# Performance work log

Hardware: AMD Instinct MI355X
Metric: run time of the kernel (lower is better)

Reference implementation:

```python
import jax, jax.numpy as jnp
import numpy as np

CODE_DIMS = [32, 32, 16]   # prod = 16384 out features
FEAT_DIM = 1024
EPS = 1e-6


def setup_inputs() -> dict:
    key = jax.random.key(0)
    kx, kw = jax.random.split(key)
    x = jax.random.normal(kx, (4, 2048, FEAT_DIM), dtype=jnp.float32)
    # per-chunk trunc-normal init like _init_weights: std = sqrt(2/(feat_dim+code_dim)), clipped at +-3 std
    parts = []
    for i, cd in enumerate(CODE_DIMS):
        std = float(np.sqrt(2.0 / (FEAT_DIM + cd)))
        parts.append(std * jax.random.truncated_normal(
            jax.random.fold_in(kw, i), -3.0, 3.0, (cd, FEAT_DIM), dtype=jnp.float32))
    weight = jnp.concatenate(parts, axis=0)  # (sum(code_dims)=80, feat_dim)
    return {"x": x, "weight": weight}


def _rms_norm(y):
    var = jnp.mean(y * y, axis=-1, keepdims=True) + EPS
    return y * jax.lax.rsqrt(var)


def reference(x, weight):
    # split weight rows into the low-rank factors
    a, b, c = jnpp_split = jnp.split(weight, np.cumsum(CODE_DIMS)[:-1].tolist(), axis=0)
    # outer product over code dims, shared feature axis z -> dynamic weight (prod(code_dims), feat_dim)
    W = jnp.einsum('az,bz,cz->abcz', a, b, c).reshape(-1, weight.shape[-1])
    y = jnp.einsum('bsi,oi->bso', x, W)  # dense projection
    return _rms_norm(y)
```

## Files before the change

### kernel.cpp

```cpp
#include <hip/hip_runtime.h>
#include <hip/hip_bf16.h>

typedef unsigned short u16;
typedef __attribute__((ext_vector_type(8))) short bf16x8;
typedef __attribute__((ext_vector_type(4))) float f32x4;
typedef __attribute__((ext_vector_type(8))) unsigned short ushort8;

#define FEAT 1024
#define NOUT 16384
#define EPS 1e-6f
#define NT 16

#define GLOBAL_AS __attribute__((address_space(1)))
#define LDS_AS __attribute__((address_space(3)))

__device__ __forceinline__ void load16_to_lds(const u16* g, u16* l) {
    __builtin_amdgcn_global_load_lds((const GLOBAL_AS void*)g, (LDS_AS void*)l, 16, 0, 0);
}

__device__ __forceinline__ u16 f32_to_bf16_bits(float f) {
    __hip_bfloat16 h = __float2bfloat16(f);
    return *reinterpret_cast<u16*>(&h);
}

__device__ __forceinline__ float bf16_bits_to_f32(u16 b) {
    unsigned u = ((unsigned)b) << 16;
    float f;
    __builtin_memcpy(&f, &u, 4);
    return f;
}

__global__ void wbuild_kernel(const float* __restrict__ w, u16* __restrict__ Wb) {
    const int t  = blockIdx.x * 256 + threadIdx.x;
    const int p  = t >> 7;
    const int k0 = (t & 127) << 3;
    const int o  = (p & ~63) | ((p & 15) << 2) | ((p >> 4) & 3);
    const int ai = o >> 9;
    const int bi = (o >> 4) & 31;
    const int ci = o & 15;
    const float* A = w + ai * FEAT + k0;
    const float* B = w + (32 + bi) * FEAT + k0;
    const float* C = w + (64 + ci) * FEAT + k0;
    ushort8 r;
#pragma unroll
    for (int j = 0; j < 8; ++j) r[j] = f32_to_bf16_bits(A[j] * B[j] * C[j]);
    *reinterpret_cast<ushort8*>(Wb + (size_t)t * 8) = r;
}

__global__ void xcast_kernel(const float* __restrict__ x, u16* __restrict__ Xb) {
    const int t = blockIdx.x * 256 + threadIdx.x;
    const float4* xv = reinterpret_cast<const float4*>(x) + (size_t)t * 2;
    const float4 f0 = xv[0];
    const float4 f1 = xv[1];
    float vals[8] = {f0.x, f0.y, f0.z, f0.w, f1.x, f1.y, f1.z, f1.w};
    ushort8 r;
#pragma unroll
    for (int j = 0; j < 8; ++j) r[j] = f32_to_bf16_bits(vals[j]);
    *reinterpret_cast<ushort8*>(Xb + (size_t)t * 8) = r;
}


#define LDSOFF(buf, isB, kh) (((buf) << 15) + ((isB) << 14) + ((kh) << 13))

#define STAGE(isB, tt, kh, buf) do {                                          \
    const u16* g = ((isB) ? gB : gA) + (size_t)(tt) * 64 + (kh) * 32 + w * 32768; \
    u16* l = lds + LDSOFF(buf, isB, kh) + w * 1024;                           \
    load16_to_lds(g, l);                                                      \
    load16_to_lds(g + 16384, l + 512);                                        \
} while (0)

#define RD_A(dst, mi, ks, buf) dst = *reinterpret_cast<const bf16x8*>(        \
    lds + LDSOFF(buf, 0, ks) + (wm * 128 + (mi) * 16 + fr) * 32 + ((kg ^ ((fr >> 1) & 3)) << 3))
#define RD_B(dst, nj, ks, buf) dst = *reinterpret_cast<const bf16x8*>(        \
    lds + LDSOFF(buf, 1, ks) + (wn * 64 + (nj) * 16 + fr) * 32 + ((kg ^ ((fr >> 1) & 3)) << 3))

#define BAR() do {                                                            \
    __builtin_amdgcn_sched_barrier(0);                                        \
    __builtin_amdgcn_s_barrier();                                             \
    __builtin_amdgcn_sched_barrier(0);                                        \
} while (0)

#define MFMAQ(mibase) do {                                                    \
    __builtin_amdgcn_s_setprio(1);                                            \
    _Pragma("unroll")                                                         \
    for (int mi = 0; mi < 4; ++mi) {                                          \
        acc[(mibase)+mi][0] = __builtin_amdgcn_mfma_f32_16x16x32_bf16(a[mi], b[0], acc[(mibase)+mi][0], 0, 0, 0); \
        acc[(mibase)+mi][1] = __builtin_amdgcn_mfma_f32_16x16x32_bf16(a[mi], b[1], acc[(mibase)+mi][1], 0, 0, 0); \
        acc[(mibase)+mi][2] = __builtin_amdgcn_mfma_f32_16x16x32_bf16(a[mi], b[2], acc[(mibase)+mi][2], 0, 0, 0); \
        acc[(mibase)+mi][3] = __builtin_amdgcn_mfma_f32_16x16x32_bf16(a[mi], b[3], acc[(mibase)+mi][3], 0, 0, 0); \
    }                                                                         \
    __builtin_amdgcn_s_setprio(0);                                            \
} while (0)

#define WAIT_H1(t) do {                                                       \
    if ((t) == NT - 1) { asm volatile("s_waitcnt vmcnt(0)" ::: "memory"); }   \
    else               { asm volatile("s_waitcnt vmcnt(8)" ::: "memory"); }   \
} while (0)
#define WAIT_H2(t) do {                                                       \
    if ((t) < NT - 2)       { asm volatile("s_waitcnt vmcnt(8)" ::: "memory"); } \
    else if ((t) == NT - 2) { asm volatile("s_waitcnt vmcnt(4)" ::: "memory"); } \
} while (0)

#define HALF(kh, buf, doStage, stT, stKh, stBuf, WAITC) do {                  \
    RD_A(a[0], 0, kh, buf); RD_A(a[1], 1, kh, buf);                           \
    RD_A(a[2], 2, kh, buf); RD_A(a[3], 3, kh, buf);                           \
    RD_B(b[0], 0, kh, buf); RD_B(b[1], 1, kh, buf);                           \
    RD_B(b[2], 2, kh, buf); RD_B(b[3], 3, kh, buf);                           \
    if (doStage) STAGE(0, stT, stKh, stBuf);                                  \
    MFMAQ(0);                                                                 \
    RD_A(a[0], 4, kh, buf); RD_A(a[1], 5, kh, buf);                           \
    RD_A(a[2], 6, kh, buf); RD_A(a[3], 7, kh, buf);                           \
    if (doStage) STAGE(1, stT, stKh, stBuf);                                  \
    MFMAQ(4);                                                                 \
    WAITC;                                                                    \
    BAR();                                                                    \
} while (0)

#define TILE_BODY(t, buf, nbuf) do {                                          \
    HALF(0, buf, (t) < NT - 1, (t) + 1, 1, nbuf, WAIT_H1(t));                 \
    HALF(1, buf, (t) < NT - 2, (t) + 2, 0, buf,  WAIT_H2(t));                 \
} while (0)

__global__ __launch_bounds__(512, 2) void gemm_kernel(const u16* __restrict__ Xb,
                                                      const u16* __restrict__ Wb,
                                                      u16* __restrict__ Y) {
    __shared__ u16 lds[65536];

    const int tid  = threadIdx.x;
    const int lane = tid & 63;
    const int w    = tid >> 6;
    const int wm   = w >> 2;
    const int wn   = w & 3;
    const int fr   = lane & 15;
    const int kg   = lane >> 4;

    const int bid = blockIdx.x;
    const int xcd = bid & 7;
    const int o   = bid >> 3;
    const int cb  = xcd * 8 + (o >> 7) * 4 + (o & 3);
    const int rb  = (o >> 2) & 31;
    const int brow = rb * 256;
    const int bcol = cb * 256;

    const int srow   = lane >> 2;
    const int kchunk = (lane & 3) ^ ((lane >> 3) & 3);
    const u16* gA = Xb + (size_t)(brow + srow) * FEAT + kchunk * 8;
    const u16* gB = Wb + (size_t)(bcol + srow) * FEAT + kchunk * 8;

    f32x4 acc[8][4] = {};
    bf16x8 a[4], b[4];

    STAGE(0, 0, 0, 0);
    STAGE(1, 0, 0, 0);
    STAGE(0, 0, 1, 0);
    STAGE(1, 0, 1, 0);
    STAGE(0, 1, 0, 1);
    STAGE(1, 1, 0, 1);
    asm volatile("s_waitcnt vmcnt(8)" ::: "memory");
    BAR();

    for (int tt = 0; tt < NT; tt += 2) {
        TILE_BODY(tt, 0, 1);
        TILE_BODY(tt + 1, 1, 0);
    }

    const int colbase = bcol + wn * 64 + fr * 4;
#pragma unroll
    for (int mi = 0; mi < 8; ++mi) {
#pragma unroll
        for (int r = 0; r < 4; ++r) {
            const int row = brow + wm * 128 + mi * 16 + kg * 4 + r;
            const unsigned lo = (unsigned)f32_to_bf16_bits(acc[mi][0][r]) |
                                ((unsigned)f32_to_bf16_bits(acc[mi][1][r]) << 16);
            const unsigned hi = (unsigned)f32_to_bf16_bits(acc[mi][2][r]) |
                                ((unsigned)f32_to_bf16_bits(acc[mi][3][r]) << 16);
            uint2 pk; pk.x = lo; pk.y = hi;
            *reinterpret_cast<uint2*>(Y + (size_t)row * 32768 + colbase) = pk;
        }
    }
}

__global__ __launch_bounds__(1024) void scale_kernel(const u16* __restrict__ Y,
                                                     float* __restrict__ out) {
    const int row = blockIdx.x;
    const int tid = threadIdx.x;
    const ushort8* yr = reinterpret_cast<const ushort8*>(Y + (size_t)row * 32768);
    const ushort8 v0 = yr[2 * tid];
    const ushort8 v1 = yr[2 * tid + 1];

    float f[16];
#pragma unroll
    for (int j = 0; j < 8; ++j) {
        f[j]     = bf16_bits_to_f32(v0[j]);
        f[8 + j] = bf16_bits_to_f32(v1[j]);
    }
    float ss = 0.f;
#pragma unroll
    for (int j = 0; j < 16; ++j) ss += f[j] * f[j];

#pragma unroll
    for (int off = 1; off < 64; off <<= 1) ss += __shfl_xor(ss, off, 64);
    __shared__ float wss[16];
    if ((tid & 63) == 0) wss[tid >> 6] = ss;
    __syncthreads();
    float tot = 0.f;
#pragma unroll
    for (int i = 0; i < 16; ++i) tot += wss[i];
    const float sc = rsqrtf(tot * (1.0f / (float)NOUT) + EPS);

    float4* orow = reinterpret_cast<float4*>(out + (size_t)row * NOUT) + tid * 4;
#pragma unroll
    for (int q = 0; q < 4; ++q) {
        float4 ov;
        ov.x = f[q * 4 + 0] * sc;
        ov.y = f[q * 4 + 1] * sc;
        ov.z = f[q * 4 + 2] * sc;
        ov.w = f[q * 4 + 3] * sc;
        orow[q] = ov;
    }
}

extern "C" void kernel_launch(void* const* d_in, const int* in_sizes, int n_in,
                              void* d_out, int out_size, void* d_ws, size_t ws_size,
                              hipStream_t stream) {
    const float* x = (const float*)d_in[0];
    const float* w = (const float*)d_in[1];
    float* out = (float*)d_out;

    const int M = in_sizes[0] / FEAT;

    u16* Wb = (u16*)d_ws;
    u16* Xb = (u16*)((char*)d_ws + (size_t)NOUT * FEAT * 2);

    u16* Y = (u16*)d_out;

    wbuild_kernel<<<(NOUT * (FEAT / 8)) / 256, 256, 0, stream>>>(w, Wb);
    xcast_kernel<<<(M * FEAT / 8) / 256, 256, 0, stream>>>(x, Xb);

    const int nblk = (M / 256) * (NOUT / 256);
    gemm_kernel<<<nblk, 512, 0, stream>>>(Xb, Wb, Y);

    scale_kernel<<<M, 1024, 0, stream>>>(Y, out);
}
```

Before: 451.7 us.

## Switch GEMM inner loop from 16x16x32 to 32x32x16 MFMA tiles

Replaces the 16x16x32 bf16 MFMA with the 32x32x16 variant. Each wave now holds 4x2 accumulators of 16 floats instead of 8x4 of 4, and fewer A/B fragments are read from LDS per step. The weight-row permutation in the build kernel and the epilogue store mapping change to match the new output layout. The aim is higher operand reuse per LDS read and fewer MFMA issues. The trade-off is narrower 4-byte stores in the epilogue and possible changes to LDS bank behaviour.

```diff
diff --git a/kernel.cpp b/kernel.cpp
--- a/kernel.cpp
+++ b/kernel.cpp
@@ -3,7 +3,7 @@
 
 typedef unsigned short u16;
 typedef __attribute__((ext_vector_type(8))) short bf16x8;
-typedef __attribute__((ext_vector_type(4))) float f32x4;
+typedef __attribute__((ext_vector_type(16))) float f32x16;
 typedef __attribute__((ext_vector_type(8))) unsigned short ushort8;
 
 #define FEAT 1024
@@ -34,7 +34,7 @@
     const int t  = blockIdx.x * 256 + threadIdx.x;
     const int p  = t >> 7;
     const int k0 = (t & 127) << 3;
-    const int o  = (p & ~63) | ((p & 15) << 2) | ((p >> 4) & 3);
+    const int o  = (p & ~63) | ((p & 31) << 1) | ((p >> 5) & 1);
     const int ai = o >> 9;
     const int bi = (o >> 4) & 31;
     const int ci = o & 15;
@@ -69,10 +69,12 @@
     load16_to_lds(g + 16384, l + 512);                                        \
 } while (0)
 
-#define RD_A(dst, mi, ks, buf) dst = *reinterpret_cast<const bf16x8*>(        \
-    lds + LDSOFF(buf, 0, ks) + (wm * 128 + (mi) * 16 + fr) * 32 + ((kg ^ ((fr >> 1) & 3)) << 3))
-#define RD_B(dst, nj, ks, buf) dst = *reinterpret_cast<const bf16x8*>(        \
-    lds + LDSOFF(buf, 1, ks) + (wn * 64 + (nj) * 16 + fr) * 32 + ((kg ^ ((fr >> 1) & 3)) << 3))
+#define RD_A(dst, mi, ks, kh, buf) dst = *reinterpret_cast<const bf16x8*>(    \
+    lds + LDSOFF(buf, 0, kh) + (wm * 128 + (mi) * 32 + fr5) * 32 +            \
+    (((((ks) * 2) + hi) ^ ((fr5 >> 1) & 3)) << 3))
+#define RD_B(dst, nt, ks, kh, buf) dst = *reinterpret_cast<const bf16x8*>(    \
+    lds + LDSOFF(buf, 1, kh) + (wn * 64 + (nt) * 32 + fr5) * 32 +             \
+    (((((ks) * 2) + hi) ^ ((fr5 >> 1) & 3)) << 3))
 
 #define BAR() do {                                                            \
     __builtin_amdgcn_sched_barrier(0);                                        \
@@ -80,14 +82,12 @@
     __builtin_amdgcn_sched_barrier(0);                                        \
 } while (0)
 
-#define MFMAQ(mibase) do {                                                    \
+#define MFMAQ() do {                                                          \
     __builtin_amdgcn_s_setprio(1);                                            \
     _Pragma("unroll")                                                         \
     for (int mi = 0; mi < 4; ++mi) {                                          \
-        acc[(mibase)+mi][0] = __builtin_amdgcn_mfma_f32_16x16x32_bf16(a[mi], b[0], acc[(mibase)+mi][0], 0, 0, 0); \
-        acc[(mibase)+mi][1] = __builtin_amdgcn_mfma_f32_16x16x32_bf16(a[mi], b[1], acc[(mibase)+mi][1], 0, 0, 0); \
-        acc[(mibase)+mi][2] = __builtin_amdgcn_mfma_f32_16x16x32_bf16(a[mi], b[2], acc[(mibase)+mi][2], 0, 0, 0); \
-        acc[(mibase)+mi][3] = __builtin_amdgcn_mfma_f32_16x16x32_bf16(a[mi], b[3], acc[(mibase)+mi][3], 0, 0, 0); \
+        acc[mi][0] = __builtin_amdgcn_mfma_f32_32x32x16_bf16(a[mi], b[0], acc[mi][0], 0, 0, 0); \
+        acc[mi][1] = __builtin_amdgcn_mfma_f32_32x32x16_bf16(a[mi], b[1], acc[mi][1], 0, 0, 0); \
     }                                                                         \
     __builtin_amdgcn_s_setprio(0);                                            \
 } while (0)
@@ -102,16 +102,16 @@
 } while (0)
 
 #define HALF(kh, buf, doStage, stT, stKh, stBuf, WAITC) do {                  \
-    RD_A(a[0], 0, kh, buf); RD_A(a[1], 1, kh, buf);                           \
-    RD_A(a[2], 2, kh, buf); RD_A(a[3], 3, kh, buf);                           \
-    RD_B(b[0], 0, kh, buf); RD_B(b[1], 1, kh, buf);                           \
-    RD_B(b[2], 2, kh, buf); RD_B(b[3], 3, kh, buf);                           \
+    RD_A(a[0], 0, 0, kh, buf); RD_A(a[1], 1, 0, kh, buf);                     \
+    RD_A(a[2], 2, 0, kh, buf); RD_A(a[3], 3, 0, kh, buf);                     \
+    RD_B(b[0], 0, 0, kh, buf); RD_B(b[1], 1, 0, kh, buf);                     \
     if (doStage) STAGE(0, stT, stKh, stBuf);                                  \
-    MFMAQ(0);                                                                 \
-    RD_A(a[0], 4, kh, buf); RD_A(a[1], 5, kh, buf);                           \
-    RD_A(a[2], 6, kh, buf); RD_A(a[3], 7, kh, buf);                           \
+    MFMAQ();                                                                  \
+    RD_A(a[0], 0, 1, kh, buf); RD_A(a[1], 1, 1, kh, buf);                     \
+    RD_A(a[2], 2, 1, kh, buf); RD_A(a[3], 3, 1, kh, buf);                     \
+    RD_B(b[0], 0, 1, kh, buf); RD_B(b[1], 1, 1, kh, buf);                     \
     if (doStage) STAGE(1, stT, stKh, stBuf);                                  \
-    MFMAQ(4);                                                                 \
+    MFMAQ();                                                                  \
     WAITC;                                                                    \
     BAR();                                                                    \
 } while (0)
@@ -131,8 +131,8 @@
     const int w    = tid >> 6;
     const int wm   = w >> 2;
     const int wn   = w & 3;
-    const int fr   = lane & 15;
-    const int kg   = lane >> 4;
+    const int fr5  = lane & 31;
+    const int hi   = lane >> 5;
 
     const int bid = blockIdx.x;
     const int xcd = bid & 7;
@@ -147,8 +147,8 @@
     const u16* gA = Xb + (size_t)(brow + srow) * FEAT + kchunk * 8;
     const u16* gB = Wb + (size_t)(bcol + srow) * FEAT + kchunk * 8;
 
-    f32x4 acc[8][4] = {};
-    bf16x8 a[4], b[4];
+    f32x16 acc[4][2] = {};
+    bf16x8 a[4], b[2];
 
     STAGE(0, 0, 0, 0);
     STAGE(1, 0, 0, 0);
@@ -164,18 +164,15 @@
         TILE_BODY(tt + 1, 1, 0);
     }
 
-    const int colbase = bcol + wn * 64 + fr * 4;
-#pragma unroll
-    for (int mi = 0; mi < 8; ++mi) {
-#pragma unroll
-        for (int r = 0; r < 4; ++r) {
-            const int row = brow + wm * 128 + mi * 16 + kg * 4 + r;
-            const unsigned lo = (unsigned)f32_to_bf16_bits(acc[mi][0][r]) |
-                                ((unsigned)f32_to_bf16_bits(acc[mi][1][r]) << 16);
-            const unsigned hi = (unsigned)f32_to_bf16_bits(acc[mi][2][r]) |
-                                ((unsigned)f32_to_bf16_bits(acc[mi][3][r]) << 16);
-            uint2 pk; pk.x = lo; pk.y = hi;
-            *reinterpret_cast<uint2*>(Y + (size_t)row * 32768 + colbase) = pk;
+    const int colbase = bcol + wn * 64 + fr5 * 2;
+#pragma unroll
+    for (int mi = 0; mi < 4; ++mi) {
+#pragma unroll
+        for (int rg = 0; rg < 16; ++rg) {
+            const int row = brow + wm * 128 + mi * 32 + (rg & 3) + 8 * (rg >> 2) + 4 * hi;
+            const unsigned pk = (unsigned)f32_to_bf16_bits(acc[mi][0][rg]) |
+                                ((unsigned)f32_to_bf16_bits(acc[mi][1][rg]) << 16);
+            *reinterpret_cast<unsigned*>(Y + (size_t)row * 32768 + colbase) = pk;
         }
     }
 }
```

Result: slower. 465.1 us (+3.0%).

## Load GEMM B operand directly from global into registers, bypassing LDS

Applied to the files above, without the earlier changes.

The weight (B) tiles are now read by each wave straight from global memory into registers with vector loads and double-buffered across k-halves. Only the X (A) tiles are still staged through LDS, so the LDS footprint is halved. The pipeline is rebuilt around this, with per-tile LDS staging of A and register prefetch of B ahead of the MFMAs. This removes LDS write/read traffic for B. In exchange, global-load latency now sits directly in front of the MFMAs, and B rows are fetched redundantly by the two wm wave groups through the cache.

```diff
diff --git a/kernel.cpp b/kernel.cpp
--- a/kernel.cpp
+++ b/kernel.cpp
@@ -60,19 +60,29 @@
 }
 
 
-#define LDSOFF(buf, isB, kh) (((buf) << 15) + ((isB) << 14) + ((kh) << 13))
-
-#define STAGE(isB, tt, kh, buf) do {                                          \
-    const u16* g = ((isB) ? gB : gA) + (size_t)(tt) * 64 + (kh) * 32 + w * 32768; \
-    u16* l = lds + LDSOFF(buf, isB, kh) + w * 1024;                           \
-    load16_to_lds(g, l);                                                      \
-    load16_to_lds(g + 16384, l + 512);                                        \
-} while (0)
-
-#define RD_A(dst, mi, ks, buf) dst = *reinterpret_cast<const bf16x8*>(        \
-    lds + LDSOFF(buf, 0, ks) + (wm * 128 + (mi) * 16 + fr) * 32 + ((kg ^ ((fr >> 1) & 3)) << 3))
-#define RD_B(dst, nj, ks, buf) dst = *reinterpret_cast<const bf16x8*>(        \
-    lds + LDSOFF(buf, 1, ks) + (wn * 64 + (nj) * 16 + fr) * 32 + ((kg ^ ((fr >> 1) & 3)) << 3))
+#define LOFF(buf, kh) ((buf) * 16384 + (kh) * 8192)
+
+#define STAGE_A(tt, buf) do {                                                 \
+    const u16* g = gA + (size_t)(tt) * 64 + (size_t)w * 32768;                \
+    u16* l0 = lds + LOFF(buf, 0) + w * 1024;                                  \
+    u16* l1 = lds + LOFF(buf, 1) + w * 1024;                                  \
+    load16_to_lds(g,             l0);                                         \
+    load16_to_lds(g + 16384,     l0 + 512);                                   \
+    load16_to_lds(g + 32,        l1);                                         \
+    load16_to_lds(g + 32 + 16384, l1 + 512);                                  \
+} while (0)
+
+#define LD_B(dst, tt, kh) do {                                                \
+    const u16* gb = gB + (size_t)(tt) * 64 + (kh) * 32;                       \
+    dst[0] = *reinterpret_cast<const bf16x8*>(gb);                            \
+    dst[1] = *reinterpret_cast<const bf16x8*>(gb + 16 * FEAT);                \
+    dst[2] = *reinterpret_cast<const bf16x8*>(gb + 32 * FEAT);                \
+    dst[3] = *reinterpret_cast<const bf16x8*>(gb + 48 * FEAT);                \
+} while (0)
+
+#define RD_A(dst, mi, mh, kh, buf) dst = *reinterpret_cast<const bf16x8*>(    \
+    lds + LOFF(buf, kh) + (wm * 128 + (mh) * 64 + (mi) * 16 + fr) * 32 +      \
+    ((kg ^ ((fr >> 1) & 3)) << 3))
 
 #define BAR() do {                                                            \
     __builtin_amdgcn_sched_barrier(0);                                        \
@@ -80,51 +90,51 @@
     __builtin_amdgcn_sched_barrier(0);                                        \
 } while (0)
 
-#define MFMAQ(mibase) do {                                                    \
+#define MFMAQ(mh, kh, buf, bb) do {                                           \
+    bf16x8 a0, a1, a2, a3;                                                    \
+    RD_A(a0, 0, mh, kh, buf); RD_A(a1, 1, mh, kh, buf);                       \
+    RD_A(a2, 2, mh, kh, buf); RD_A(a3, 3, mh, kh, buf);                       \
     __builtin_amdgcn_s_setprio(1);                                            \
-    _Pragma("unroll")                                                         \
-    for (int mi = 0; mi < 4; ++mi) {                                          \
-        acc[(mibase)+mi][0] = __builtin_amdgcn_mfma_f32_16x16x32_bf16(a[mi], b[0], acc[(mibase)+mi][0], 0, 0, 0); \
-        acc[(mibase)+mi][1] = __builtin_amdgcn_mfma_f32_16x16x32_bf16(a[mi], b[1], acc[(mibase)+mi][1], 0, 0, 0); \
-        acc[(mibase)+mi][2] = __builtin_amdgcn_mfma_f32_16x16x32_bf16(a[mi], b[2], acc[(mibase)+mi][2], 0, 0, 0); \
-        acc[(mibase)+mi][3] = __builtin_amdgcn_mfma_f32_16x16x32_bf16(a[mi], b[3], acc[(mibase)+mi][3], 0, 0, 0); \
+    acc[(mh)*4+0][0] = __builtin_amdgcn_mfma_f32_16x16x32_bf16(a0, bb[0], acc[(mh)*4+0][0], 0, 0, 0); \
+    acc[(mh)*4+0][1] = __builtin_amdgcn_mfma_f32_16x16x32_bf16(a0, bb[1], acc[(mh)*4+0][1], 0, 0, 0); \
+    acc[(mh)*4+0][2] = __builtin_amdgcn_mfma_f32_16x16x32_bf16(a0, bb[2], acc[(mh)*4+0][2], 0, 0, 0); \
+    acc[(mh)*4+0][3] = __builtin_amdgcn_mfma_f32_16x16x32_bf16(a0, bb[3], acc[(mh)*4+0][3], 0, 0, 0); \
+    acc[(mh)*4+1][0] = __builtin_amdgcn_mfma_f32_16x16x32_bf16(a1, bb[0], acc[(mh)*4+1][0], 0, 0, 0); \
+    acc[(mh)*4+1][1] = __builtin_amdgcn_mfma_f32_16x16x32_bf16(a1, bb[1], acc[(mh)*4+1][1], 0, 0, 0); \
+    acc[(mh)*4+1][2] = __builtin_amdgcn_mfma_f32_16x16x32_bf16(a1, bb[2], acc[(mh)*4+1][2], 0, 0, 0); \
+    acc[(mh)*4+1][3] = __builtin_amdgcn_mfma_f32_16x16x32_bf16(a1, bb[3], acc[(mh)*4+1][3], 0, 0, 0); \
+    acc[(mh)*4+2][0] = __builtin_amdgcn_mfma_f32_16x16x32_bf16(a2, bb[0], acc[(mh)*4+2][0], 0, 0, 0); \
+    acc[(mh)*4+2][1] = __builtin_amdgcn_mfma_f32_16x16x32_bf16(a2, bb[1], acc[(mh)*4+2][1], 0, 0, 0); \
+    acc[(mh)*4+2][2] = __builtin_amdgcn_mfma_f32_16x16x32_bf16(a2, bb[2], acc[(mh)*4+2][2], 0, 0, 0); \
+    acc[(mh)*4+2][3] = __builtin_amdgcn_mfma_f32_16x16x32_bf16(a2, bb[3], acc[(mh)*4+2][3], 0, 0, 0); \
+    acc[(mh)*4+3][0] = __builtin_amdgcn_mfma_f32_16x16x32_bf16(a3, bb[0], acc[(mh)*4+3][0], 0, 0, 0); \
+    acc[(mh)*4+3][1] = __builtin_amdgcn_mfma_f32_16x16x32_bf16(a3, bb[1], acc[(mh)*4+3][1], 0, 0, 0); \
+    acc[(mh)*4+3][2] = __builtin_amdgcn_mfma_f32_16x16x32_bf16(a3, bb[2], acc[(mh)*4+3][2], 0, 0, 0); \
+    acc[(mh)*4+3][3] = __builtin_amdgcn_mfma_f32_16x16x32_bf16(a3, bb[3], acc[(mh)*4+3][3], 0, 0, 0); \
+    __builtin_amdgcn_s_setprio(0);                                            \
+} while (0)
+
+#define TILE(t, buf, nbuf) do {                                               \
+    LD_B(bOdd, t, 1);                                                         \
+    __builtin_amdgcn_sched_barrier(0);                                        \
+    if ((t) >= 1 && (t) < NT - 1) STAGE_A((t) + 1, nbuf);                     \
+    __builtin_amdgcn_sched_barrier(0);                                        \
+    MFMAQ(0, 0, buf, bEven);                                                  \
+    MFMAQ(1, 0, buf, bEven);                                                  \
+    if ((t) < NT - 1) LD_B(bEven, (t) + 1, 0);                                \
+    __builtin_amdgcn_sched_barrier(0);                                        \
+    MFMAQ(0, 1, buf, bOdd);                                                   \
+    MFMAQ(1, 1, buf, bOdd);                                                   \
+    if ((t) < NT - 1) {                                                       \
+        asm volatile("s_waitcnt vmcnt(4)" ::: "memory");                      \
+        BAR();                                                                \
     }                                                                         \
-    __builtin_amdgcn_s_setprio(0);                                            \
-} while (0)
-
-#define WAIT_H1(t) do {                                                       \
-    if ((t) == NT - 1) { asm volatile("s_waitcnt vmcnt(0)" ::: "memory"); }   \
-    else               { asm volatile("s_waitcnt vmcnt(8)" ::: "memory"); }   \
-} while (0)
-#define WAIT_H2(t) do {                                                       \
-    if ((t) < NT - 2)       { asm volatile("s_waitcnt vmcnt(8)" ::: "memory"); } \
-    else if ((t) == NT - 2) { asm volatile("s_waitcnt vmcnt(4)" ::: "memory"); } \
-} while (0)
-
-#define HALF(kh, buf, doStage, stT, stKh, stBuf, WAITC) do {                  \
-    RD_A(a[0], 0, kh, buf); RD_A(a[1], 1, kh, buf);                           \
-    RD_A(a[2], 2, kh, buf); RD_A(a[3], 3, kh, buf);                           \
-    RD_B(b[0], 0, kh, buf); RD_B(b[1], 1, kh, buf);                           \
-    RD_B(b[2], 2, kh, buf); RD_B(b[3], 3, kh, buf);                           \
-    if (doStage) STAGE(0, stT, stKh, stBuf);                                  \
-    MFMAQ(0);                                                                 \
-    RD_A(a[0], 4, kh, buf); RD_A(a[1], 5, kh, buf);                           \
-    RD_A(a[2], 6, kh, buf); RD_A(a[3], 7, kh, buf);                           \
-    if (doStage) STAGE(1, stT, stKh, stBuf);                                  \
-    MFMAQ(4);                                                                 \
-    WAITC;                                                                    \
-    BAR();                                                                    \
-} while (0)
-
-#define TILE_BODY(t, buf, nbuf) do {                                          \
-    HALF(0, buf, (t) < NT - 1, (t) + 1, 1, nbuf, WAIT_H1(t));                 \
-    HALF(1, buf, (t) < NT - 2, (t) + 2, 0, buf,  WAIT_H2(t));                 \
 } while (0)
 
 __global__ __launch_bounds__(512, 2) void gemm_kernel(const u16* __restrict__ Xb,
                                                       const u16* __restrict__ Wb,
                                                       u16* __restrict__ Y) {
-    __shared__ u16 lds[65536];
+    __shared__ u16 lds[32768];
 
     const int tid  = threadIdx.x;
     const int lane = tid & 63;
@@ -145,23 +155,20 @@
     const int srow   = lane >> 2;
     const int kchunk = (lane & 3) ^ ((lane >> 3) & 3);
     const u16* gA = Xb + (size_t)(brow + srow) * FEAT + kchunk * 8;
-    const u16* gB = Wb + (size_t)(bcol + srow) * FEAT + kchunk * 8;
+    const u16* gB = Wb + (size_t)(bcol + wn * 64 + fr) * FEAT + kg * 8;
 
     f32x4 acc[8][4] = {};
-    bf16x8 a[4], b[4];
-
-    STAGE(0, 0, 0, 0);
-    STAGE(1, 0, 0, 0);
-    STAGE(0, 0, 1, 0);
-    STAGE(1, 0, 1, 0);
-    STAGE(0, 1, 0, 1);
-    STAGE(1, 1, 0, 1);
+    bf16x8 bEven[4], bOdd[4];
+
+    STAGE_A(0, 0);
+    STAGE_A(1, 1);
+    LD_B(bEven, 0, 0);
     asm volatile("s_waitcnt vmcnt(8)" ::: "memory");
     BAR();
 
     for (int tt = 0; tt < NT; tt += 2) {
-        TILE_BODY(tt, 0, 1);
-        TILE_BODY(tt + 1, 1, 0);
+        TILE(tt, 0, 1);
+        TILE(tt + 1, 1, 0);
     }
 
     const int colbase = bcol + wn * 64 + fr * 4;
```

After: 527.3 us. 16.7% more time.

## Shrink GEMM tile to 256x128 with K=32 stages for higher occupancy

Applied to the files above, without the earlier changes.

Restructures the bf16 GEMM from 256x256 output tiles with two K-halves per 64-wide stage to 256x128 tiles with simple 32-wide K stages, double-buffered at a prefetch distance of two. Each wave now computes a 64x64 subtile. LDS use drops from 128 KB to 48 KB per block and launch bounds request 4 blocks per CU, so more blocks can stay resident to hide latency. In exchange, arithmetic intensity per tile is lower, B reuse is halved, and there are twice as many barriers per K of work.

```diff
diff --git a/kernel.cpp b/kernel.cpp
--- a/kernel.cpp
+++ b/kernel.cpp
@@ -9,7 +9,7 @@
 #define FEAT 1024
 #define NOUT 16384
 #define EPS 1e-6f
-#define NT 16
+#define NT 32
 
 #define GLOBAL_AS __attribute__((address_space(1)))
 #define LDS_AS __attribute__((address_space(3)))
@@ -60,19 +60,20 @@
 }
 
 
-#define LDSOFF(buf, isB, kh) (((buf) << 15) + ((isB) << 14) + ((kh) << 13))
-
-#define STAGE(isB, tt, kh, buf) do {                                          \
-    const u16* g = ((isB) ? gB : gA) + (size_t)(tt) * 64 + (kh) * 32 + w * 32768; \
-    u16* l = lds + LDSOFF(buf, isB, kh) + w * 1024;                           \
-    load16_to_lds(g, l);                                                      \
-    load16_to_lds(g + 16384, l + 512);                                        \
+#define LA(buf) (lds + (buf) * 12288)
+#define LB(buf) (lds + (buf) * 12288 + 8192)
+
+#define STAGE(tt, buf) do {                                                   \
+    const int ko = (tt) * 32;                                                 \
+    load16_to_lds(gA0 + ko, LA(buf) + w * 512);                               \
+    load16_to_lds(gA1 + ko, LA(buf) + 4096 + w * 512);                        \
+    load16_to_lds(gB0 + ko, LB(buf) + w * 512);                               \
 } while (0)
 
-#define RD_A(dst, mi, ks, buf) dst = *reinterpret_cast<const bf16x8*>(        \
-    lds + LDSOFF(buf, 0, ks) + (wm * 128 + (mi) * 16 + fr) * 32 + ((kg ^ ((fr >> 1) & 3)) << 3))
-#define RD_B(dst, nj, ks, buf) dst = *reinterpret_cast<const bf16x8*>(        \
-    lds + LDSOFF(buf, 1, ks) + (wn * 64 + (nj) * 16 + fr) * 32 + ((kg ^ ((fr >> 1) & 3)) << 3))
+#define RD_A(dst, mi, buf) dst = *reinterpret_cast<const bf16x8*>(            \
+    LA(buf) + (wm * 64 + (mi) * 16 + fr) * 32 + ((kg ^ ((fr >> 1) & 3)) << 3))
+#define RD_B(dst, nj, buf) dst = *reinterpret_cast<const bf16x8*>(            \
+    LB(buf) + (wn * 64 + (nj) * 16 + fr) * 32 + ((kg ^ ((fr >> 1) & 3)) << 3))
 
 #define BAR() do {                                                            \
     __builtin_amdgcn_sched_barrier(0);                                        \
@@ -80,96 +81,85 @@
     __builtin_amdgcn_sched_barrier(0);                                        \
 } while (0)
 
-#define MFMAQ(mibase) do {                                                    \
+#define TILE(t, buf) do {                                                     \
+    bf16x8 a0, a1, a2, a3, b0, b1, b2, b3;                                    \
+    RD_A(a0, 0, buf); RD_A(a1, 1, buf); RD_A(a2, 2, buf); RD_A(a3, 3, buf);   \
+    RD_B(b0, 0, buf); RD_B(b1, 1, buf); RD_B(b2, 2, buf); RD_B(b3, 3, buf);   \
     __builtin_amdgcn_s_setprio(1);                                            \
-    _Pragma("unroll")                                                         \
-    for (int mi = 0; mi < 4; ++mi) {                                          \
-        acc[(mibase)+mi][0] = __builtin_amdgcn_mfma_f32_16x16x32_bf16(a[mi], b[0], acc[(mibase)+mi][0], 0, 0, 0); \
-        acc[(mibase)+mi][1] = __builtin_amdgcn_mfma_f32_16x16x32_bf16(a[mi], b[1], acc[(mibase)+mi][1], 0, 0, 0); \
-        acc[(mibase)+mi][2] = __builtin_amdgcn_mfma_f32_16x16x32_bf16(a[mi], b[2], acc[(mibase)+mi][2], 0, 0, 0); \
-        acc[(mibase)+mi][3] = __builtin_amdgcn_mfma_f32_16x16x32_bf16(a[mi], b[3], acc[(mibase)+mi][3], 0, 0, 0); \
+    acc[0][0] = __builtin_amdgcn_mfma_f32_16x16x32_bf16(a0, b0, acc[0][0], 0, 0, 0); \
+    acc[0][1] = __builtin_amdgcn_mfma_f32_16x16x32_bf16(a0, b1, acc[0][1], 0, 0, 0); \
+    acc[0][2] = __builtin_amdgcn_mfma_f32_16x16x32_bf16(a0, b2, acc[0][2], 0, 0, 0); \
+    acc[0][3] = __builtin_amdgcn_mfma_f32_16x16x32_bf16(a0, b3, acc[0][3], 0, 0, 0); \
+    acc[1][0] = __builtin_amdgcn_mfma_f32_16x16x32_bf16(a1, b0, acc[1][0], 0, 0, 0); \
+    acc[1][1] = __builtin_amdgcn_mfma_f32_16x16x32_bf16(a1, b1, acc[1][1], 0, 0, 0); \
+    acc[1][2] = __builtin_amdgcn_mfma_f32_16x16x32_bf16(a1, b2, acc[1][2], 0, 0, 0); \
+    acc[1][3] = __builtin_amdgcn_mfma_f32_16x16x32_bf16(a1, b3, acc[1][3], 0, 0, 0); \
+    acc[2][0] = __builtin_amdgcn_mfma_f32_16x16x32_bf16(a2, b0, acc[2][0], 0, 0, 0); \
+    acc[2][1] = __builtin_amdgcn_mfma_f32_16x16x32_bf16(a2, b1, acc[2][1], 0, 0, 0); \
+    acc[2][2] = __builtin_amdgcn_mfma_f32_16x16x32_bf16(a2, b2, acc[2][2], 0, 0, 0); \
+    acc[2][3] = __builtin_amdgcn_mfma_f32_16x16x32_bf16(a2, b3, acc[2][3], 0, 0, 0); \
+    acc[3][0] = __builtin_amdgcn_mfma_f32_16x16x32_bf16(a3, b0, acc[3][0], 0, 0, 0); \
+    acc[3][1] = __builtin_amdgcn_mfma_f32_16x16x32_bf16(a3, b1, acc[3][1], 0, 0, 0); \
+    acc[3][2] = __builtin_amdgcn_mfma_f32_16x16x32_bf16(a3, b2, acc[3][2], 0, 0, 0); \
+    acc[3][3] = __builtin_amdgcn_mfma_f32_16x16x32_bf16(a3, b3, acc[3][3], 0, 0, 0); \
+    __builtin_amdgcn_s_setprio(0);                                            \
+    if ((t) < NT - 1) {                                                       \
+        BAR();                                                                \
+        if ((t) < NT - 2) {                                                   \
+            STAGE((t) + 2, buf);                                              \
+            asm volatile("s_waitcnt vmcnt(3)" ::: "memory");                  \
+        } else {                                                              \
+            asm volatile("s_waitcnt vmcnt(0)" ::: "memory");                  \
+        }                                                                     \
+        BAR();                                                                \
     }                                                                         \
-    __builtin_amdgcn_s_setprio(0);                                            \
 } while (0)
 
-#define WAIT_H1(t) do {                                                       \
-    if ((t) == NT - 1) { asm volatile("s_waitcnt vmcnt(0)" ::: "memory"); }   \
-    else               { asm volatile("s_waitcnt vmcnt(8)" ::: "memory"); }   \
-} while (0)
-#define WAIT_H2(t) do {                                                       \
-    if ((t) < NT - 2)       { asm volatile("s_waitcnt vmcnt(8)" ::: "memory"); } \
-    else if ((t) == NT - 2) { asm volatile("s_waitcnt vmcnt(4)" ::: "memory"); } \
-} while (0)
-
-#define HALF(kh, buf, doStage, stT, stKh, stBuf, WAITC) do {                  \
-    RD_A(a[0], 0, kh, buf); RD_A(a[1], 1, kh, buf);                           \
-    RD_A(a[2], 2, kh, buf); RD_A(a[3], 3, kh, buf);                           \
-    RD_B(b[0], 0, kh, buf); RD_B(b[1], 1, kh, buf);                           \
-    RD_B(b[2], 2, kh, buf); RD_B(b[3], 3, kh, buf);                           \
-    if (doStage) STAGE(0, stT, stKh, stBuf);                                  \
-    MFMAQ(0);                                                                 \
-    RD_A(a[0], 4, kh, buf); RD_A(a[1], 5, kh, buf);                           \
-    RD_A(a[2], 6, kh, buf); RD_A(a[3], 7, kh, buf);                           \
-    if (doStage) STAGE(1, stT, stKh, stBuf);                                  \
-    MFMAQ(4);                                                                 \
-    WAITC;                                                                    \
-    BAR();                                                                    \
-} while (0)
-
-#define TILE_BODY(t, buf, nbuf) do {                                          \
-    HALF(0, buf, (t) < NT - 1, (t) + 1, 1, nbuf, WAIT_H1(t));                 \
-    HALF(1, buf, (t) < NT - 2, (t) + 2, 0, buf,  WAIT_H2(t));                 \
-} while (0)
-
-__global__ __launch_bounds__(512, 2) void gemm_kernel(const u16* __restrict__ Xb,
+__global__ __launch_bounds__(512, 4) void gemm_kernel(const u16* __restrict__ Xb,
                                                       const u16* __restrict__ Wb,
                                                       u16* __restrict__ Y) {
-    __shared__ u16 lds[65536];
+    __shared__ u16 lds[24576];
 
     const int tid  = threadIdx.x;
     const int lane = tid & 63;
     const int w    = tid >> 6;
-    const int wm   = w >> 2;
-    const int wn   = w & 3;
+    const int wm   = w >> 1;
+    const int wn   = w & 1;
     const int fr   = lane & 15;
     const int kg   = lane >> 4;
 
     const int bid = blockIdx.x;
     const int xcd = bid & 7;
     const int o   = bid >> 3;
-    const int cb  = xcd * 8 + (o >> 7) * 4 + (o & 3);
+    const int cb  = xcd * 16 + (o >> 7) * 4 + (o & 3);
     const int rb  = (o >> 2) & 31;
     const int brow = rb * 256;
-    const int bcol = cb * 256;
-
-    const int srow   = lane >> 2;
-    const int kchunk = (lane & 3) ^ ((lane >> 3) & 3);
-    const u16* gA = Xb + (size_t)(brow + srow) * FEAT + kchunk * 8;
-    const u16* gB = Wb + (size_t)(bcol + srow) * FEAT + kchunk * 8;
-
-    f32x4 acc[8][4] = {};
-    bf16x8 a[4], b[4];
-
-    STAGE(0, 0, 0, 0);
-    STAGE(1, 0, 0, 0);
-    STAGE(0, 0, 1, 0);
-    STAGE(1, 0, 1, 0);
-    STAGE(0, 1, 0, 1);
-    STAGE(1, 1, 0, 1);
-    asm volatile("s_waitcnt vmcnt(8)" ::: "memory");
+    const int bcol = cb * 128;
+
+    const int srow = tid >> 2;
+    const int kc   = (tid & 3) ^ ((srow >> 1) & 3);
+    const u16* gA0 = Xb + (size_t)(brow + srow) * FEAT + kc * 8;
+    const u16* gA1 = gA0 + 128 * FEAT;
+    const u16* gB0 = Wb + (size_t)(bcol + srow) * FEAT + kc * 8;
+
+    f32x4 acc[4][4] = {};
+
+    STAGE(0, 0);
+    STAGE(1, 1);
+    asm volatile("s_waitcnt vmcnt(3)" ::: "memory");
     BAR();
 
-    for (int tt = 0; tt < NT; tt += 2) {
-        TILE_BODY(tt, 0, 1);
-        TILE_BODY(tt + 1, 1, 0);
+#pragma unroll 2
+    for (int tt = 0; tt < NT; ++tt) {
+        TILE(tt, (tt & 1));
     }
 
     const int colbase = bcol + wn * 64 + fr * 4;
 #pragma unroll
-    for (int mi = 0; mi < 8; ++mi) {
+    for (int mi = 0; mi < 4; ++mi) {
 #pragma unroll
         for (int r = 0; r < 4; ++r) {
-            const int row = brow + wm * 128 + mi * 16 + kg * 4 + r;
+            const int row = brow + wm * 64 + mi * 16 + kg * 4 + r;
             const unsigned lo = (unsigned)f32_to_bf16_bits(acc[mi][0][r]) |
                                 ((unsigned)f32_to_bf16_bits(acc[mi][1][r]) << 16);
             const unsigned hi = (unsigned)f32_to_bf16_bits(acc[mi][2][r]) |
@@ -237,7 +227,7 @@
     wbuild_kernel<<<(NOUT * (FEAT / 8)) / 256, 256, 0, stream>>>(w, Wb);
     xcast_kernel<<<(M * FEAT / 8) / 256, 256, 0, stream>>>(x, Xb);
 
-    const int nblk = (M / 256) * (NOUT / 256);
+    const int nblk = (M / 256) * (NOUT / 128);
     gemm_kernel<<<nblk, 512, 0, stream>>>(Xb, Wb, Y);
 
     scale_kernel<<<M, 1024, 0, stream>>>(Y, out);
```

Result: slower. 466.9 us (+3.4%).
